# Kernel tuning notes

Measured on AMD Instinct MI355X. Metric: run time of the kernel, lower is better.

The kernel has to match this reference:

```python
import jax, jax.numpy as jnp
import numpy as np
from jax import lax

B = 256
NUM_CLASSES = 10
IN_CAPS = 32 * 6 * 6  # 1152
IN_DIM = 8
OUT_DIM = 16
NUM_ITERS = 3


def squash(t, axis=-1):
    sq = jnp.sum(t * t, axis=axis, keepdims=True)
    return (sq / (1.0 + sq)) * t / jnp.sqrt(sq)


def conv2d(x, w, b, stride):
    y = lax.conv_general_dilated(x, w, (stride, stride), 'VALID',
                                 dimension_numbers=('NCHW', 'OIHW', 'NCHW'))
    return y + b[None, :, None, None]


def setup_inputs() -> dict:
    key = jax.random.key(0)
    ks = jax.random.split(key, 12)
    f = jnp.float32
    return {
        'x': jax.random.uniform(ks[0], (B, 1, 28, 28), dtype=f),
        'conv1_w': jax.random.normal(ks[1], (256, 1, 9, 9), dtype=f) * 0.05,
        'conv1_b': jnp.zeros((256,), dtype=f),
        'prim_w': jax.random.normal(ks[2], (IN_DIM * 32, 256, 9, 9), dtype=f) * 0.02,
        'prim_b': jnp.zeros((IN_DIM * 32,), dtype=f),
        'route_w': jax.random.normal(ks[3], (NUM_CLASSES, IN_CAPS, IN_DIM, OUT_DIM), dtype=f),
        'dec_w1': jax.random.normal(ks[4], (OUT_DIM * NUM_CLASSES, 512), dtype=f) * 0.05,
        'dec_b1': jnp.zeros((512,), dtype=f),
        'dec_w2': jax.random.normal(ks[5], (512, 1024), dtype=f) * 0.04,
        'dec_b2': jnp.zeros((1024,), dtype=f),
        'dec_w3': jax.random.normal(ks[6], (1024, 28 * 28), dtype=f) * 0.03,
        'dec_b3': jnp.zeros((28 * 28,), dtype=f),
    }


def reference(x, conv1_w, conv1_b, prim_w, prim_b, route_w,
              dec_w1, dec_b1, dec_w2, dec_b2, dec_w3, dec_b3):
    bsz = x.shape[0]
    # conv1 + relu -> [B,256,20,20]
    h = jax.nn.relu(conv2d(x, conv1_w, conv1_b, 1))
    # primary capsules: 8 parallel convs (stacked into one) -> [B, 8*32, 6, 6]
    p = conv2d(h, prim_w, prim_b, 2)
    # each capsule conv flattens to [B, 32*36], concatenated along last dim
    p = p.reshape(bsz, IN_DIM, 32 * 6 * 6).transpose(0, 2, 1)  # [B, 1152, 8]
    u = squash(p, axis=-1)
    # priors: [o, b, i, d_out]
    priors = jnp.einsum('bic,oicd->obid', u, route_w)
    # routing by agreement: softmax over in_capsules (dim i), per original code
    logits = jnp.zeros((NUM_CLASSES, bsz, IN_CAPS, 1), dtype=priors.dtype)
    outputs = None
    for it in range(NUM_ITERS):
        probs = jax.nn.softmax(logits, axis=2)              # [o,b,i,1]
        outputs = squash(jnp.sum(probs * priors, axis=2, keepdims=True))  # [o,b,1,d]
        if it != NUM_ITERS - 1:
            logits = logits + jnp.sum(priors * outputs, axis=-1, keepdims=True)
    vecs = outputs.reshape(NUM_CLASSES, bsz, OUT_DIM).transpose(1, 0, 2)  # [B,10,16]
    classes = jnp.sqrt(jnp.sum(vecs * vecs, axis=-1))
    classes = jax.nn.softmax(classes, axis=1)               # [B,10]
    # y=None path: one-hot of predicted class (non-differentiable mask)
    y = jax.nn.one_hot(jnp.argmax(classes, axis=1), NUM_CLASSES, dtype=vecs.dtype)
    dec_in = (vecs * y[:, :, None]).reshape(bsz, -1)        # [B,160]
    hdec = jax.nn.relu(dec_in @ dec_w1 + dec_b1)
    hdec = jax.nn.relu(hdec @ dec_w2 + dec_b2)
    reconstruction = jax.nn.sigmoid(hdec @ dec_w3 + dec_b3)  # [B,784]
    return classes, reconstruction
```

## Files before the change

kernel.cpp:

```cpp
#include <hip/hip_runtime.h>
#include <hip/hip_bf16.h>
#include <math.h>


typedef __attribute__((ext_vector_type(8))) short bf16x8;
typedef __attribute__((ext_vector_type(4))) float f32x4;

__device__ __forceinline__ void gl16(const void* g, void* l) {
  __builtin_amdgcn_global_load_lds((const __attribute__((address_space(1))) void*)g,
                                   (__attribute__((address_space(3))) void*)l,
                                   16, 0, 0);
}

__global__ __launch_bounds__(256) void k_conv1(const float* __restrict__ x,
                                               const float* __restrict__ w,
                                               const float* __restrict__ bias,
                                               __hip_bfloat16* __restrict__ hT) {
  const int bid = blockIdx.x;
  const int img = bid >> 2, ocq = bid & 3;
  __shared__ float xs[784];
  __shared__ float ws[64 * 81];
  __shared__ __attribute__((aligned(16))) __hip_bfloat16 tile[8 * 1288];
  const int t = threadIdx.x;
  const float4* xg = (const float4*)(x + (size_t)img * 784);
  if (t < 196) ((float4*)xs)[t] = xg[t];
  const float4* wg = (const float4*)(w + (size_t)ocq * 64 * 81);
  for (int i = t; i < 1296; i += 256) ((float4*)ws)[i] = wg[i];
  __syncthreads();
  const int ocl = t & 63, rowg = t >> 6;
  const int oc = ocq * 64 + ocl;
  const int chl = ocl >> 3, icl = ocl & 7;
  const float bv = bias[oc];
  __hip_bfloat16* hb = hT + ((size_t)img * 32 + ocq * 8) * 6560;
#pragma unroll 1
  for (int it = 0; it < 5; it++) {
    const int r = it * 4 + rowg;
    float acc[20];
#pragma unroll
    for (int p = 0; p < 20; p++) acc[p] = bv;
#pragma unroll
    for (int ky = 0; ky < 9; ky++) {
      float xr[28];
      const float* xrow = &xs[(r + ky) * 28];
#pragma unroll
      for (int q = 0; q < 7; q++) ((float4*)xr)[q] = ((const float4*)xrow)[q];
      float wr[9];
#pragma unroll
      for (int i = 0; i < 9; i++) wr[i] = ws[ocl * 81 + ky * 9 + i];
#pragma unroll
      for (int kx = 0; kx < 9; kx++)
#pragma unroll
        for (int p = 0; p < 20; p++)
          acc[p] = fmaf(wr[kx], xr[p + kx], acc[p]);
    }
#pragma unroll
    for (int p = 0; p < 20; p++) {
      const float v = fmaxf(acc[p], 0.f);
      const __hip_bfloat16 hi = __float2bfloat16(v);
      const __hip_bfloat16 lo = __float2bfloat16(v - __bfloat162float(hi));
      tile[chl * 1288 + (p * 8 + rowg * 2) * 8 + icl] = hi;
      tile[chl * 1288 + (p * 8 + rowg * 2 + 1) * 8 + icl] = lo;
    }
    __syncthreads();
#pragma unroll
    for (int q = 0; q < 5; q++) {
      const int idx = q * 256 + t;
      const int c2 = idx / 160, rem = idx - c2 * 160;
      const int xx = rem >> 3, j = rem & 7;
      const float4 vdat = *(const float4*)&tile[c2 * 1288 + rem * 8];
      *(float4*)(hb + (size_t)c2 * 6560 + (size_t)(xx * 41 + it * 8 + j) * 8) = vdat;
    }
    __syncthreads();
  }
}

__global__ __launch_bounds__(256) void k_wrep(const float* __restrict__ pw,
                                              __hip_bfloat16* __restrict__ wGp) {
  const int s = blockIdx.x >> 2, ocq = blockIdx.x & 3;
  const int ch = s / 21, tq = s - ch * 21;
  __hip_bfloat16* outp = wGp + ((size_t)s * 4 + ocq) * 4608;
  const int t = threadIdx.x;
  for (int e = t; e < 2048; e += 256) {
    const int ocl = e >> 5, k = e & 31;
    const int tapl = k >> 3, icl = k & 7;
    const int tap = tq * 4 + tapl, ic = ch * 8 + icl;
    const int oc = ocq * 64 + ocl;
    const float v = (tap < 81) ? pw[((size_t)oc * 256 + ic) * 81 + tap] : 0.f;
    const __hip_bfloat16 hi = __float2bfloat16(v);
    const __hip_bfloat16 lo = __float2bfloat16(v - __bfloat162float(hi));
    outp[ocl * 72 + k] = hi;
    outp[ocl * 72 + 32 + k] = lo;
  }
  for (int e = t; e < 512; e += 256) {
    const int ocl = e >> 3, j = e & 7;
    outp[ocl * 72 + 64 + j] = __float2bfloat16(0.f);
  }
}

__global__ __launch_bounds__(256) void k_rrep(const float* __restrict__ rw,
                                              float* __restrict__ rwT) {
  const int o = blockIdx.x / 18, ig = blockIdx.x % 18;
  __shared__ float tile[64 * 129];
  const int t = threadIdx.x;
  for (int idx = t; idx < 64 * 128; idx += 256) {
    const int i = idx >> 7, cd = idx & 127;
    tile[i * 129 + cd] = rw[((size_t)o * 1152 + ig * 64 + i) * 128 + cd];
  }
  __syncthreads();
  for (int idx = t; idx < 64 * 128; idx += 256) {
    const int cd = idx >> 6, il = idx & 63;
    rwT[((size_t)o * 128 + cd) * 1152 + ig * 64 + il] = tile[il * 129 + cd];
  }
}

#define HT_B 52480
#define PQ_F 2359296
__global__ __launch_bounds__(512) void k_conv2(
    const __hip_bfloat16* __restrict__ hTg,
    const __hip_bfloat16* __restrict__ wGp,
    float* __restrict__ pq, int c0) {
  __shared__ char hT[HT_B];
  const int bid = blockIdx.x;
  int ig, ocq, kq;
  if (gridDim.x == 512) {
    ig = (bid & 7) | (((bid >> 5) & 7) << 3);
    ocq = (bid >> 3) & 3;
    kq = bid >> 8;
  } else {
    ig = bid >> 3;
    ocq = (bid >> 1) & 3;
    kq = bid & 1;
  }
  const int t = threadIdx.x;
  const int w = t >> 6, lane = t & 63;
  const int lquad = lane >> 4, lrow = lane & 15;
  const int mhalf = w >> 2;
  const int nt = mhalf ? 4 : 5;
  const int mtb = mhalf ? 5 : 0;
  const int ocg = ocq * 64 + (w & 3) * 16 + lrow;
  int abase[5];
#pragma unroll
  for (int i = 0; i < 5; i++) {
    int m = (mtb + i) * 16 + lrow;
    if (i >= nt) m = 0;
    const int img = m / 36, px = m - img * 36;
    const int oy = px / 6, ox = px - oy * 6;
    abase[i] = img * 13120 + ox * 1312 + oy * 64;
  }
  f32x4 acc[5];
#pragma unroll
  for (int i = 0; i < 5; i++) acc[i] = (f32x4){0.f, 0.f, 0.f, 0.f};

  const char* hgc = (const char*)hTg;
  const char* wp = (const char*)wGp + ((size_t)(kq * 336) * 4 + ocq) * 4608 +
                   ((w & 3) * 16 + lrow) * 144 + lquad * 16;
  bf16x8 bh = *(const bf16x8*)wp;
  bf16x8 bl = *(const bf16x8*)(wp + 64);
  wp += 18432;
#pragma unroll 1
  for (int chl = 0; chl < 16; chl++) {
    const int ch = kq * 16 + chl;
    const char* hch = hgc + ((size_t)(ig * 128) + ch) * 13120;
#pragma unroll
    for (int rr = 0; rr < 6; rr++) {
      const int idx = t + rr * 512;
      const int j = idx / 820, r = idx - j * 820;
      gl16(hch + (size_t)j * 419840 + r * 16, hT + rr * 8192 + w * 1024);
    }
    if (t < 208) {
      const int idx = 3072 + t;
      const int j = idx / 820, r = idx - j * 820;
      gl16(hch + (size_t)j * 419840 + r * 16, hT + 49152 + w * 1024);
    }
    __syncthreads();
#pragma unroll 1
    for (int tq = 0; tq < 21; tq++) {
      const bf16x8 nh = *(const bf16x8*)wp;
      const bf16x8 nl = *(const bf16x8*)(wp + 64);
      wp += 18432;
      const int tt = tq * 4 + lquad;
      const int ky = tt / 9, kx = tt - ky * 9;
      const int toff = kx * 656 + ky * 32;
      bf16x8 ah[5];
#pragma unroll
      for (int i = 0; i < 5; i++)
        ah[i] = *(const bf16x8*)(hT + abase[i] + toff);
#pragma unroll
      for (int i = 0; i < 5; i++)
        if (i < nt) acc[i] = __builtin_amdgcn_mfma_f32_16x16x32_bf16(ah[i], bh, acc[i], 0, 0, 0);
#pragma unroll
      for (int i = 0; i < 5; i++)
        if (i < nt) acc[i] = __builtin_amdgcn_mfma_f32_16x16x32_bf16(ah[i], bl, acc[i], 0, 0, 0);
      bf16x8 al[5];
#pragma unroll
      for (int i = 0; i < 5; i++)
        al[i] = *(const bf16x8*)(hT + abase[i] + toff + 16);
#pragma unroll
      for (int i = 0; i < 5; i++)
        if (i < nt) acc[i] = __builtin_amdgcn_mfma_f32_16x16x32_bf16(al[i], bh, acc[i], 0, 0, 0);
      bh = nh;
      bl = nl;
    }
    __syncthreads();
  }
  float* pblk = pq + (size_t)kq * PQ_F;
#pragma unroll
  for (int i = 0; i < 5; i++) {
    if (i < nt) {
#pragma unroll
      for (int r = 0; r < 4; r++) {
        const int m = (mtb + i) * 16 + lquad * 4 + r;
        const int img = m / 36, px = m - img * 36;
        pblk[((size_t)(c0 + ig * 4 + img) * 36 + px) * 256 + ocg] = acc[i][r];
      }
    }
  }
}

__global__ __launch_bounds__(256) void k_squash(const float* __restrict__ pq,
                                                const float* __restrict__ bias,
                                                float* __restrict__ u) {
  const int b = blockIdx.x;
  __shared__ float ps[36 * 257];
  const int t = threadIdx.x;
  const float4* s0 = (const float4*)(pq + (size_t)b * 9216);
  const float4* s1 = (const float4*)(pq + (size_t)PQ_F + (size_t)b * 9216);
#pragma unroll
  for (int q = 0; q < 9; q++) {
    const int idx = q * 256 + t;
    const float4 a = s0[idx], c = s1[idx];
    const int px = idx >> 6, oc = (idx & 63) * 4;
    float* dst = &ps[px * 257 + oc];
    dst[0] = a.x + c.x; dst[1] = a.y + c.y;
    dst[2] = a.z + c.z; dst[3] = a.w + c.w;
  }
  __syncthreads();
#pragma unroll
  for (int rr = 0; rr < 5; rr++) {
    const int i = rr * 256 + t;
    if (i < 1152) {
      const int cp = i / 36, px = i - cp * 36;
      float s[8], sq = 0.f;
#pragma unroll
      for (int d = 0; d < 8; d++) {
        s[d] = ps[px * 257 + d * 32 + cp] + bias[d * 32 + cp];
        sq = fmaf(s[d], s[d], sq);
      }
      const float scale = sq / ((1.f + sq) * sqrtf(sq));
      float o[8];
#pragma unroll
      for (int d = 0; d < 8; d++) o[d] = s[d] * scale;
      float* ub = u + ((size_t)b * 1152 + i) * 8;
      ((float4*)ub)[0] = ((float4*)o)[0];
      ((float4*)ub)[1] = ((float4*)o)[1];
    }
  }
}

__device__ __forceinline__ float wsum(float v) {
#pragma unroll
  for (int o = 32; o > 0; o >>= 1) v += __shfl_xor(v, o, 64);
  return v;
}
__device__ __forceinline__ float wmaxr(float v) {
#pragma unroll
  for (int o = 32; o > 0; o >>= 1) v = fmaxf(v, __shfl_xor(v, o, 64));
  return v;
}

__global__ __launch_bounds__(512) void k_route(const float* __restrict__ u,
                                               const float* __restrict__ rwT,
                                               float* __restrict__ vecs) {
  const int bid = blockIdx.x;
  int o, b;
  if (bid < 2048) { o = bid & 7; b = bid >> 3; }
  else { const int ix = bid - 2048; o = 8 + (ix & 1); b = ix >> 1; }
  __shared__ __attribute__((aligned(16))) float pri4[4 * 1152 * 4];
  __shared__ float red[8 * 17];
  __shared__ float redm[8];
  const int t = threadIdx.x;
  const int wave = t >> 6, lane = t & 63;
  const float* ub = u + (size_t)b * 9216;
  const float* rwo = rwT + (size_t)o * 128 * 1152;
#pragma unroll
  for (int ci = 0; ci < 3; ci++) {
    const bool valid = (ci < 2) || (t < 128);
    const int i = valid ? (t + ci * 512) : 0;
    float uv[8];
    *(float4*)&uv[0] = *(const float4*)(ub + i * 8);
    *(float4*)&uv[4] = *(const float4*)(ub + i * 8 + 4);
    float a[16];
#pragma unroll
    for (int d = 0; d < 16; d++) a[d] = 0.f;
#pragma unroll
    for (int c = 0; c < 8; c++) {
      const float* wcol = rwo + (size_t)(c * 16) * 1152 + i;
#pragma unroll
      for (int d = 0; d < 16; d++)
        a[d] = fmaf(uv[c], wcol[(size_t)d * 1152], a[d]);
    }
    if (valid) {
#pragma unroll
      for (int q = 0; q < 4; q++)
        *(float4*)&pri4[(q * 1152 + i) * 4] = *(float4*)&a[q * 4];
    }
  }
  __syncthreads();
  float l[3];
#pragma unroll
  for (int ci = 0; ci < 3; ci++)
    l[ci] = ((ci < 2) || (t < 128)) ? 0.f : -1e30f;
  float v[16];
#pragma unroll 1
  for (int it = 0; it < 3; it++) {
    float m = fmaxf(fmaxf(l[0], l[1]), l[2]);
    m = wmaxr(m);
    if (lane == 0) redm[wave] = m;
    __syncthreads();
    m = redm[0];
#pragma unroll
    for (int wv2 = 1; wv2 < 8; wv2++) m = fmaxf(m, redm[wv2]);
    float Z = 0.f, S[16];
#pragma unroll
    for (int d = 0; d < 16; d++) S[d] = 0.f;
#pragma unroll
    for (int ci = 0; ci < 3; ci++) {
      const bool valid = (ci < 2) || (t < 128);
      const int i = valid ? (t + ci * 512) : 0;
      const float e = expf(l[ci] - m);
      Z += e;
#pragma unroll
      for (int q = 0; q < 4; q++) {
        const float4 p4 = *(const float4*)&pri4[(q * 1152 + i) * 4];
        S[q * 4 + 0] = fmaf(e, p4.x, S[q * 4 + 0]);
        S[q * 4 + 1] = fmaf(e, p4.y, S[q * 4 + 1]);
        S[q * 4 + 2] = fmaf(e, p4.z, S[q * 4 + 2]);
        S[q * 4 + 3] = fmaf(e, p4.w, S[q * 4 + 3]);
      }
    }
    Z = wsum(Z);
#pragma unroll
    for (int d = 0; d < 16; d++) S[d] = wsum(S[d]);
    __syncthreads();
    if (lane == 0) {
      red[wave * 17] = Z;
#pragma unroll
      for (int d = 0; d < 16; d++) red[wave * 17 + 1 + d] = S[d];
    }
    __syncthreads();
    float Zt = 0.f;
#pragma unroll
    for (int wv2 = 0; wv2 < 8; wv2++) Zt += red[wv2 * 17];
    float sv[16], sq = 0.f;
#pragma unroll
    for (int d = 0; d < 16; d++) {
      float sd = 0.f;
#pragma unroll
      for (int wv2 = 0; wv2 < 8; wv2++) sd += red[wv2 * 17 + 1 + d];
      sd /= Zt;
      sv[d] = sd;
      sq = fmaf(sd, sd, sq);
    }
    const float scale = sq / ((1.f + sq) * sqrtf(sq));
#pragma unroll
    for (int d = 0; d < 16; d++) v[d] = scale * sv[d];
    if (it < 2) {
#pragma unroll
      for (int ci = 0; ci < 3; ci++) {
        const bool valid = (ci < 2) || (t < 128);
        const int i = valid ? (t + ci * 512) : 0;
        float dot = 0.f;
#pragma unroll
        for (int q = 0; q < 4; q++) {
          const float4 p4 = *(const float4*)&pri4[(q * 1152 + i) * 4];
          dot = fmaf(p4.x, v[q * 4 + 0], dot);
          dot = fmaf(p4.y, v[q * 4 + 1], dot);
          dot = fmaf(p4.z, v[q * 4 + 2], dot);
          dot = fmaf(p4.w, v[q * 4 + 3], dot);
        }
        l[ci] += dot;
      }
      __syncthreads();
    }
  }
  if (t == 0) {
    float* vb = vecs + ((size_t)b * 10 + o) * 16;
#pragma unroll
    for (int d = 0; d < 16; d++) vb[d] = v[d];
  }
}

__global__ __launch_bounds__(64) void k_cls(const float* __restrict__ vecs,
                                            float* __restrict__ out,
                                            float* __restrict__ selvec,
                                            int* __restrict__ amv) {
  const int b = blockIdx.x, t = threadIdx.x;
  __shared__ float vbs[160];
  __shared__ float nrm[10];
  __shared__ int ams;
  const float* vb = vecs + (size_t)b * 160;
  for (int idx = t; idx < 160; idx += 64) vbs[idx] = vb[idx];
  __syncthreads();
  if (t < 10) {
    float sq = 0.f;
#pragma unroll
    for (int d = 0; d < 16; d++) { const float xv = vbs[t * 16 + d]; sq = fmaf(xv, xv, sq); }
    nrm[t] = sqrtf(sq);
  }
  __syncthreads();
  if (t == 0) {
    float m = nrm[0];
#pragma unroll
    for (int o = 1; o < 10; o++) m = fmaxf(m, nrm[o]);
    float e[10], Z = 0.f;
#pragma unroll
    for (int o = 0; o < 10; o++) { e[o] = expf(nrm[o] - m); Z += e[o]; }
    const float inv = 1.f / Z;
    int am = 0;
    float best = e[0] * inv;
#pragma unroll
    for (int o = 0; o < 10; o++) {
      const float c = e[o] * inv;
      out[(size_t)b * 10 + o] = c;
      if (o > 0 && c > best) { best = c; am = o; }
    }
    amv[b] = am;
    ams = am;
  }
  __syncthreads();
  if (t < 16) selvec[(size_t)b * 16 + t] = vbs[ams * 16 + t];
}

__global__ __launch_bounds__(512) void k_dec1(const float* __restrict__ selvec,
                                              const int* __restrict__ amv,
                                              const float* __restrict__ w1,
                                              const float* __restrict__ b1,
                                              float* __restrict__ h1) {
  const int b = blockIdx.x, t = threadIdx.x;
  __shared__ float sv[16];
  __shared__ int ams;
  if (t < 16) sv[t] = selvec[(size_t)b * 16 + t];
  if (t == 0) ams = amv[b];
  __syncthreads();
  const float* wrow = w1 + (size_t)ams * 16 * 512;
  float acc = b1[t];
#pragma unroll
  for (int d = 0; d < 16; d++) acc = fmaf(sv[d], wrow[d * 512 + t], acc);
  h1[(size_t)b * 512 + t] = fmaxf(acc, 0.f);
}

__global__ __launch_bounds__(128) void k_dec2(const float* __restrict__ h1,
                                              const float* __restrict__ w2,
                                              const float* __restrict__ b2,
                                              float* __restrict__ h2) {
  const int nc = blockIdx.x >> 7, bg = blockIdx.x & 127;
  const int t = threadIdx.x;
  const int n = nc * 128 + t;
  const int bs = bg * 2;
  __shared__ float h1s[2 * 512];
  __shared__ float wts[32 * 128];
  {
    const float4* src = (const float4*)(h1 + (size_t)bs * 512);
    for (int i = t; i < 256; i += 128) ((float4*)h1s)[i] = src[i];
  }
  float acc[2];
  const float bb = b2[n];
  acc[0] = bb; acc[1] = bb;
#pragma unroll 1
  for (int kt = 0; kt < 16; kt++) {
    __syncthreads();
#pragma unroll
    for (int r = 0; r < 32; r++)
      wts[r * 128 + t] = w2[(size_t)(kt * 32 + r) * 1024 + n];
    __syncthreads();
#pragma unroll
    for (int k4 = 0; k4 < 8; k4++) {
      float wq[4];
#pragma unroll
      for (int q = 0; q < 4; q++) wq[q] = wts[(k4 * 4 + q) * 128 + t];
#pragma unroll
      for (int j = 0; j < 2; j++) {
        const float4 hv = *(const float4*)&h1s[j * 512 + kt * 32 + k4 * 4];
        acc[j] = fmaf(hv.x, wq[0], acc[j]);
        acc[j] = fmaf(hv.y, wq[1], acc[j]);
        acc[j] = fmaf(hv.z, wq[2], acc[j]);
        acc[j] = fmaf(hv.w, wq[3], acc[j]);
      }
    }
  }
#pragma unroll
  for (int j = 0; j < 2; j++) h2[(size_t)(bs + j) * 1024 + n] = fmaxf(acc[j], 0.f);
}

__global__ __launch_bounds__(128) void k_dec3(const float* __restrict__ h2,
                                              const float* __restrict__ w3,
                                              const float* __restrict__ b3,
                                              float* __restrict__ out) {
  const int nc = blockIdx.x >> 7, bg = blockIdx.x & 127;
  const int t = threadIdx.x;
  const int bs = bg * 2;
  __shared__ float h2s[2 * 1024];
  __shared__ float wts[32 * 112];
  {
    const float4* src = (const float4*)(h2 + (size_t)bs * 1024);
    for (int i = t; i < 512; i += 128) ((float4*)h2s)[i] = src[i];
  }
  const int n = nc * 112 + (t < 112 ? t : 0);
  float acc[2];
  const float bb = b3[n];
  acc[0] = bb; acc[1] = bb;
#pragma unroll 1
  for (int kt = 0; kt < 32; kt++) {
    __syncthreads();
#pragma unroll
    for (int r = 0; r < 32; r++)
      if (t < 112) wts[r * 112 + t] = w3[(size_t)(kt * 32 + r) * 784 + n];
    __syncthreads();
    if (t < 112) {
#pragma unroll
      for (int k4 = 0; k4 < 8; k4++) {
        float wq[4];
#pragma unroll
        for (int q = 0; q < 4; q++) wq[q] = wts[(k4 * 4 + q) * 112 + t];
#pragma unroll
        for (int j = 0; j < 2; j++) {
          const float4 hv = *(const float4*)&h2s[j * 1024 + kt * 32 + k4 * 4];
          acc[j] = fmaf(hv.x, wq[0], acc[j]);
          acc[j] = fmaf(hv.y, wq[1], acc[j]);
          acc[j] = fmaf(hv.z, wq[2], acc[j]);
          acc[j] = fmaf(hv.w, wq[3], acc[j]);
        }
      }
    }
  }
  if (t < 112) {
#pragma unroll
    for (int j = 0; j < 2; j++)
      out[(size_t)(bs + j) * 784 + n] = 1.f / (1.f + expf(-acc[j]));
  }
}

extern "C" void kernel_launch(void* const* d_in, const int* in_sizes, int n_in,
                              void* d_out, int out_size, void* d_ws, size_t ws_size,
                              hipStream_t stream) {
  const float* x   = (const float*)d_in[0];
  const float* c1w = (const float*)d_in[1];
  const float* c1b = (const float*)d_in[2];
  const float* pw  = (const float*)d_in[3];
  const float* pb  = (const float*)d_in[4];
  const float* rw  = (const float*)d_in[5];
  const float* w1  = (const float*)d_in[6];
  const float* b1  = (const float*)d_in[7];
  const float* w2  = (const float*)d_in[8];
  const float* b2  = (const float*)d_in[9];
  const float* w3  = (const float*)d_in[10];
  const float* b3  = (const float*)d_in[11];
  float* out = (float*)d_out;
  float* ws = (float*)d_ws;

  const size_t WGP_F = ((size_t)672 * 4 * 4608 + 18432) / 4;
  const size_t U_F = 2359296;
  const size_t RWT_F = 10 * 128 * 1152;
  const size_t SMALL_F = 40960 + 4096 + 256 + 131072 + 262144;
  const size_t fixed_f = WGP_F + 2 * PQ_F + U_F + RWT_F + SMALL_F;
  int chunk = 256;
  while (chunk > 8 && (fixed_f + (size_t)chunk * 104960) * 4 > ws_size) chunk >>= 1;

  __hip_bfloat16* wGp  = (__hip_bfloat16*)ws;
  __hip_bfloat16* hTgc = (__hip_bfloat16*)(ws + WGP_F);
  float* pq   = ws + WGP_F + (size_t)chunk * 104960;
  float* u    = pq + 2 * PQ_F;
  float* rwT  = u + U_F;
  float* vecs = rwT + RWT_F;
  float* sel  = vecs + 40960;
  int*   amv  = (int*)(sel + 4096);
  float* h1   = sel + 4096 + 256;
  float* h2   = h1 + 131072;

  k_wrep<<<dim3(2688), dim3(256), 0, stream>>>(pw, wGp);
  k_rrep<<<dim3(180), dim3(256), 0, stream>>>(rw, rwT);
  for (int c0 = 0; c0 < 256; c0 += chunk) {
    k_conv1<<<dim3(chunk * 4), dim3(256), 0, stream>>>(x + (size_t)c0 * 784, c1w, c1b, hTgc);
    k_conv2<<<dim3((chunk / 4) * 8), dim3(512), 0, stream>>>(hTgc, wGp, pq, c0);
  }
  k_squash<<<dim3(256), dim3(256), 0, stream>>>(pq, pb, u);
  k_route<<<dim3(2560), dim3(512), 0, stream>>>(u, rwT, vecs);
  k_cls<<<dim3(256), dim3(64), 0, stream>>>(vecs, out, sel, amv);
  k_dec1<<<dim3(256), dim3(512), 0, stream>>>(sel, amv, w1, b1, h1);
  k_dec2<<<dim3(1024), dim3(128), 0, stream>>>(h1, w2, b2, h2);
  k_dec3<<<dim3(896), dim3(128), 0, stream>>>(h2, w3, b3, out + 2560);
}
```

Measured before the change: 808.9 us.

## Route two batch items per block and fuse classifier into decoder layer one

The routing kernel now computes priors and runs dynamic routing for two batch samples per block. Each route weight load is reused for both samples, which halves global/L2 weight traffic and the block count. The LDS footprint doubles per block and register pressure rises. The classification softmax/argmax kernel is merged into the first decoder kernel, removing a launch and the intermediate selected-vector buffers.

```diff
diff --git a/kernel.cpp b/kernel.cpp
--- a/kernel.cpp
+++ b/kernel.cpp
@@ -272,143 +272,174 @@
                                                const float* __restrict__ rwT,
                                                float* __restrict__ vecs) {
   const int bid = blockIdx.x;
-  int o, b;
-  if (bid < 2048) { o = bid & 7; b = bid >> 3; }
-  else { const int ix = bid - 2048; o = 8 + (ix & 1); b = ix >> 1; }
-  __shared__ __attribute__((aligned(16))) float pri4[4 * 1152 * 4];
-  __shared__ float red[8 * 17];
-  __shared__ float redm[8];
+  int o, bp;
+  if (bid < 1024) { o = bid & 7; bp = bid >> 3; }
+  else { const int ix = bid - 1024; o = 8 + (ix & 1); bp = ix >> 1; }
+  const int b0 = bp * 2;
+  __shared__ __attribute__((aligned(16))) float pri4[2][4608 * 4];
+  __shared__ float red[2][8 * 17];
+  __shared__ float redm[2][8];
   const int t = threadIdx.x;
   const int wave = t >> 6, lane = t & 63;
-  const float* ub = u + (size_t)b * 9216;
   const float* rwo = rwT + (size_t)o * 128 * 1152;
+  const float* ub0 = u + (size_t)b0 * 9216;
+  const float* ub1 = ub0 + 9216;
 #pragma unroll
   for (int ci = 0; ci < 3; ci++) {
     const bool valid = (ci < 2) || (t < 128);
     const int i = valid ? (t + ci * 512) : 0;
-    float uv[8];
-    *(float4*)&uv[0] = *(const float4*)(ub + i * 8);
-    *(float4*)&uv[4] = *(const float4*)(ub + i * 8 + 4);
-    float a[16];
-#pragma unroll
-    for (int d = 0; d < 16; d++) a[d] = 0.f;
+    float uv0[8], uv1[8];
+    *(float4*)&uv0[0] = *(const float4*)(ub0 + i * 8);
+    *(float4*)&uv0[4] = *(const float4*)(ub0 + i * 8 + 4);
+    *(float4*)&uv1[0] = *(const float4*)(ub1 + i * 8);
+    *(float4*)&uv1[4] = *(const float4*)(ub1 + i * 8 + 4);
+    float a0[16], a1[16];
+#pragma unroll
+    for (int d = 0; d < 16; d++) { a0[d] = 0.f; a1[d] = 0.f; }
 #pragma unroll
     for (int c = 0; c < 8; c++) {
       const float* wcol = rwo + (size_t)(c * 16) * 1152 + i;
 #pragma unroll
-      for (int d = 0; d < 16; d++)
-        a[d] = fmaf(uv[c], wcol[(size_t)d * 1152], a[d]);
+      for (int d = 0; d < 16; d++) {
+        const float wv = wcol[(size_t)d * 1152];
+        a0[d] = fmaf(uv0[c], wv, a0[d]);
+        a1[d] = fmaf(uv1[c], wv, a1[d]);
+      }
     }
     if (valid) {
 #pragma unroll
-      for (int q = 0; q < 4; q++)
-        *(float4*)&pri4[(q * 1152 + i) * 4] = *(float4*)&a[q * 4];
+      for (int q = 0; q < 4; q++) {
+        *(float4*)&pri4[0][(q * 1152 + i) * 4] = *(float4*)&a0[q * 4];
+        *(float4*)&pri4[1][(q * 1152 + i) * 4] = *(float4*)&a1[q * 4];
+      }
     }
   }
   __syncthreads();
-  float l[3];
-#pragma unroll
-  for (int ci = 0; ci < 3; ci++)
-    l[ci] = ((ci < 2) || (t < 128)) ? 0.f : -1e30f;
-  float v[16];
+  float l0[3], l1[3];
+#pragma unroll
+  for (int ci = 0; ci < 3; ci++) {
+    const float init = ((ci < 2) || (t < 128)) ? 0.f : -1e30f;
+    l0[ci] = init; l1[ci] = init;
+  }
+  float v0[16], v1[16];
 #pragma unroll 1
   for (int it = 0; it < 3; it++) {
-    float m = fmaxf(fmaxf(l[0], l[1]), l[2]);
-    m = wmaxr(m);
-    if (lane == 0) redm[wave] = m;
-    __syncthreads();
-    m = redm[0];
-#pragma unroll
-    for (int wv2 = 1; wv2 < 8; wv2++) m = fmaxf(m, redm[wv2]);
-    float Z = 0.f, S[16];
-#pragma unroll
-    for (int d = 0; d < 16; d++) S[d] = 0.f;
+    float m0 = wmaxr(fmaxf(fmaxf(l0[0], l0[1]), l0[2]));
+    float m1 = wmaxr(fmaxf(fmaxf(l1[0], l1[1]), l1[2]));
+    if (lane == 0) { redm[0][wave] = m0; redm[1][wave] = m1; }
+    __syncthreads();
+    m0 = redm[0][0]; m1 = redm[1][0];
+#pragma unroll
+    for (int wv2 = 1; wv2 < 8; wv2++) {
+      m0 = fmaxf(m0, redm[0][wv2]);
+      m1 = fmaxf(m1, redm[1][wv2]);
+    }
+    float Z0 = 0.f, Z1 = 0.f, S0[16], S1[16];
+#pragma unroll
+    for (int d = 0; d < 16; d++) { S0[d] = 0.f; S1[d] = 0.f; }
 #pragma unroll
     for (int ci = 0; ci < 3; ci++) {
       const bool valid = (ci < 2) || (t < 128);
       const int i = valid ? (t + ci * 512) : 0;
-      const float e = expf(l[ci] - m);
-      Z += e;
+      const float e0 = expf(l0[ci] - m0);
+      const float e1 = expf(l1[ci] - m1);
+      Z0 += e0; Z1 += e1;
 #pragma unroll
       for (int q = 0; q < 4; q++) {
-        const float4 p4 = *(const float4*)&pri4[(q * 1152 + i) * 4];
-        S[q * 4 + 0] = fmaf(e, p4.x, S[q * 4 + 0]);
-        S[q * 4 + 1] = fmaf(e, p4.y, S[q * 4 + 1]);
-        S[q * 4 + 2] = fmaf(e, p4.z, S[q * 4 + 2]);
-        S[q * 4 + 3] = fmaf(e, p4.w, S[q * 4 + 3]);
-      }
-    }
-    Z = wsum(Z);
-#pragma unroll
-    for (int d = 0; d < 16; d++) S[d] = wsum(S[d]);
+        const float4 p0 = *(const float4*)&pri4[0][(q * 1152 + i) * 4];
+        const float4 p1 = *(const float4*)&pri4[1][(q * 1152 + i) * 4];
+        S0[q * 4 + 0] = fmaf(e0, p0.x, S0[q * 4 + 0]);
+        S0[q * 4 + 1] = fmaf(e0, p0.y, S0[q * 4 + 1]);
+        S0[q * 4 + 2] = fmaf(e0, p0.z, S0[q * 4 + 2]);
+        S0[q * 4 + 3] = fmaf(e0, p0.w, S0[q * 4 + 3]);
+        S1[q * 4 + 0] = fmaf(e1, p1.x, S1[q * 4 + 0]);
+        S1[q * 4 + 1] = fmaf(e1, p1.y, S1[q * 4 + 1]);
+        S1[q * 4 + 2] = fmaf(e1, p1.z, S1[q * 4 + 2]);
+        S1[q * 4 + 3] = fmaf(e1, p1.w, S1[q * 4 + 3]);
+      }
+    }
+    Z0 = wsum(Z0); Z1 = wsum(Z1);
+#pragma unroll
+    for (int d = 0; d < 16; d++) { S0[d] = wsum(S0[d]); S1[d] = wsum(S1[d]); }
     __syncthreads();
     if (lane == 0) {
-      red[wave * 17] = Z;
-#pragma unroll
-      for (int d = 0; d < 16; d++) red[wave * 17 + 1 + d] = S[d];
-    }
-    __syncthreads();
-    float Zt = 0.f;
-#pragma unroll
-    for (int wv2 = 0; wv2 < 8; wv2++) Zt += red[wv2 * 17];
-    float sv[16], sq = 0.f;
+      red[0][wave * 17] = Z0; red[1][wave * 17] = Z1;
+#pragma unroll
+      for (int d = 0; d < 16; d++) {
+        red[0][wave * 17 + 1 + d] = S0[d];
+        red[1][wave * 17 + 1 + d] = S1[d];
+      }
+    }
+    __syncthreads();
+    float Zt0 = 0.f, Zt1 = 0.f;
+#pragma unroll
+    for (int wv2 = 0; wv2 < 8; wv2++) { Zt0 += red[0][wv2 * 17]; Zt1 += red[1][wv2 * 17]; }
+    float sq0 = 0.f, sq1 = 0.f;
 #pragma unroll
     for (int d = 0; d < 16; d++) {
-      float sd = 0.f;
-#pragma unroll
-      for (int wv2 = 0; wv2 < 8; wv2++) sd += red[wv2 * 17 + 1 + d];
-      sd /= Zt;
-      sv[d] = sd;
-      sq = fmaf(sd, sd, sq);
-    }
-    const float scale = sq / ((1.f + sq) * sqrtf(sq));
-#pragma unroll
-    for (int d = 0; d < 16; d++) v[d] = scale * sv[d];
+      float sd0 = 0.f, sd1 = 0.f;
+#pragma unroll
+      for (int wv2 = 0; wv2 < 8; wv2++) {
+        sd0 += red[0][wv2 * 17 + 1 + d];
+        sd1 += red[1][wv2 * 17 + 1 + d];
+      }
+      sd0 /= Zt0; sd1 /= Zt1;
+      v0[d] = sd0; v1[d] = sd1;
+      sq0 = fmaf(sd0, sd0, sq0);
+      sq1 = fmaf(sd1, sd1, sq1);
+    }
+    const float sc0 = sq0 / ((1.f + sq0) * sqrtf(sq0));
+    const float sc1 = sq1 / ((1.f + sq1) * sqrtf(sq1));
+#pragma unroll
+    for (int d = 0; d < 16; d++) { v0[d] *= sc0; v1[d] *= sc1; }
     if (it < 2) {
 #pragma unroll
       for (int ci = 0; ci < 3; ci++) {
         const bool valid = (ci < 2) || (t < 128);
         const int i = valid ? (t + ci * 512) : 0;
-        float dot = 0.f;
+        float d0 = 0.f, d1 = 0.f;
 #pragma unroll
         for (int q = 0; q < 4; q++) {
-          const float4 p4 = *(const float4*)&pri4[(q * 1152 + i) * 4];
-          dot = fmaf(p4.x, v[q * 4 + 0], dot);
-          dot = fmaf(p4.y, v[q * 4 + 1], dot);
-          dot = fmaf(p4.z, v[q * 4 + 2], dot);
-          dot = fmaf(p4.w, v[q * 4 + 3], dot);
+          const float4 p0 = *(const float4*)&pri4[0][(q * 1152 + i) * 4];
+          const float4 p1 = *(const float4*)&pri4[1][(q * 1152 + i) * 4];
+          d0 = fmaf(p0.x, v0[q * 4 + 0], d0); d0 = fmaf(p0.y, v0[q * 4 + 1], d0);
+          d0 = fmaf(p0.z, v0[q * 4 + 2], d0); d0 = fmaf(p0.w, v0[q * 4 + 3], d0);
+          d1 = fmaf(p1.x, v1[q * 4 + 0], d1); d1 = fmaf(p1.y, v1[q * 4 + 1], d1);
+          d1 = fmaf(p1.z, v1[q * 4 + 2], d1); d1 = fmaf(p1.w, v1[q * 4 + 3], d1);
         }
-        l[ci] += dot;
-      }
-      __syncthreads();
+        l0[ci] += d0; l1[ci] += d1;
+      }
     }
   }
   if (t == 0) {
-    float* vb = vecs + ((size_t)b * 10 + o) * 16;
-#pragma unroll
-    for (int d = 0; d < 16; d++) vb[d] = v[d];
-  }
-}
-
-__global__ __launch_bounds__(64) void k_cls(const float* __restrict__ vecs,
-                                            float* __restrict__ out,
-                                            float* __restrict__ selvec,
-                                            int* __restrict__ amv) {
+    float* vb0 = vecs + ((size_t)b0 * 10 + o) * 16;
+    float* vb1 = vecs + ((size_t)(b0 + 1) * 10 + o) * 16;
+#pragma unroll
+    for (int d = 0; d < 16; d++) { vb0[d] = v0[d]; vb1[d] = v1[d]; }
+  }
+}
+
+__global__ __launch_bounds__(512) void k_dec1(const float* __restrict__ vecs,
+                                              const float* __restrict__ w1,
+                                              const float* __restrict__ b1,
+                                              float* __restrict__ out,
+                                              float* __restrict__ h1) {
   const int b = blockIdx.x, t = threadIdx.x;
   __shared__ float vbs[160];
-  __shared__ float nrm[10];
+  __shared__ float sv[16];
   __shared__ int ams;
   const float* vb = vecs + (size_t)b * 160;
-  for (int idx = t; idx < 160; idx += 64) vbs[idx] = vb[idx];
-  __syncthreads();
-  if (t < 10) {
-    float sq = 0.f;
-#pragma unroll
-    for (int d = 0; d < 16; d++) { const float xv = vbs[t * 16 + d]; sq = fmaf(xv, xv, sq); }
-    nrm[t] = sqrtf(sq);
-  }
+  if (t < 160) vbs[t] = vb[t];
   __syncthreads();
   if (t == 0) {
+    float nrm[10];
+#pragma unroll
+    for (int o = 0; o < 10; o++) {
+      float sq = 0.f;
+#pragma unroll
+      for (int d = 0; d < 16; d++) { const float xv = vbs[o * 16 + d]; sq = fmaf(xv, xv, sq); }
+      nrm[o] = sqrtf(sq);
+    }
     float m = nrm[0];
 #pragma unroll
     for (int o = 1; o < 10; o++) m = fmaxf(m, nrm[o]);
@@ -424,25 +455,13 @@
       out[(size_t)b * 10 + o] = c;
       if (o > 0 && c > best) { best = c; am = o; }
     }
-    amv[b] = am;
     ams = am;
   }
   __syncthreads();
-  if (t < 16) selvec[(size_t)b * 16 + t] = vbs[ams * 16 + t];
-}
-
-__global__ __launch_bounds__(512) void k_dec1(const float* __restrict__ selvec,
-                                              const int* __restrict__ amv,
-                                              const float* __restrict__ w1,
-                                              const float* __restrict__ b1,
-                                              float* __restrict__ h1) {
-  const int b = blockIdx.x, t = threadIdx.x;
-  __shared__ float sv[16];
-  __shared__ int ams;
-  if (t < 16) sv[t] = selvec[(size_t)b * 16 + t];
-  if (t == 0) ams = amv[b];
+  const int am2 = ams;
+  if (t < 16) sv[t] = vbs[am2 * 16 + t];
   __syncthreads();
-  const float* wrow = w1 + (size_t)ams * 16 * 512;
+  const float* wrow = w1 + (size_t)am2 * 16 * 512;
   float acc = b1[t];
 #pragma unroll
   for (int d = 0; d < 16; d++) acc = fmaf(sv[d], wrow[d * 512 + t], acc);
@@ -572,9 +591,7 @@
   float* u    = pq + 2 * PQ_F;
   float* rwT  = u + U_F;
   float* vecs = rwT + RWT_F;
-  float* sel  = vecs + 40960;
-  int*   amv  = (int*)(sel + 4096);
-  float* h1   = sel + 4096 + 256;
+  float* h1   = vecs + 40960 + 4096 + 256;
   float* h2   = h1 + 131072;
 
   k_wrep<<<dim3(2688), dim3(256), 0, stream>>>(pw, wGp);
@@ -584,9 +601,8 @@
     k_conv2<<<dim3((chunk / 4) * 8), dim3(512), 0, stream>>>(hTgc, wGp, pq, c0);
   }
   k_squash<<<dim3(256), dim3(256), 0, stream>>>(pq, pb, u);
-  k_route<<<dim3(2560), dim3(512), 0, stream>>>(u, rwT, vecs);
-  k_cls<<<dim3(256), dim3(64), 0, stream>>>(vecs, out, sel, amv);
-  k_dec1<<<dim3(256), dim3(512), 0, stream>>>(sel, amv, w1, b1, h1);
+  k_route<<<dim3(1280), dim3(512), 0, stream>>>(u, rwT, vecs);
+  k_dec1<<<dim3(256), dim3(512), 0, stream>>>(vecs, w1, b1, out, h1);
   k_dec2<<<dim3(1024), dim3(128), 0, stream>>>(h1, w2, b2, h2);
   k_dec3<<<dim3(896), dim3(128), 0, stream>>>(h2, w3, b3, out + 2560);
 }
```

Result: faster. 767.9 us (-5.1%).
